# Optimization experiments

Hardware: AMD Instinct MI355X
Metric: run time of the kernel (lower is better)

The kernel has to match this reference:

```python
import jax, jax.numpy as jnp
import numpy as np
import math

B, D, L, H, K, CONV_N = 32, 128, 1024, 8, 7, 4
DK = D // H
EPS = 1e-5


def make_pos_encoding():
    i = np.arange(D, dtype=np.float64)
    freqs = np.where(i % 2 == 0, 10000.0 ** (-i / D), -(10000.0 ** ((1 - i) / D)))
    phases = np.where(i % 2 == 0, 0.0, math.pi / 2)
    pos = np.arange(L, dtype=np.float64)[None, :]  # [1, L]
    pe = np.sin(pos * freqs[:, None] + phases[:, None])  # [D, L]
    return jnp.asarray(pe, dtype=jnp.float32)


def layer_norm_2d(x, w, b):
    # nn.LayerNorm([D, L]) on [B, D, L]: normalize jointly over last two dims
    mu = jnp.mean(x, axis=(1, 2), keepdims=True)
    var = jnp.var(x, axis=(1, 2), keepdims=True)
    return (x - mu) * jax.lax.rsqrt(var + EPS) * w[None] + b[None]


def setup_inputs():
    key = jax.random.key(0)
    ks = jax.random.split(key, 24)
    s = 0.05
    x = jax.random.normal(ks[0], (B, D, L), jnp.float32)
    lengths = jax.random.randint(ks[1], (B,), L // 2, L + 1)
    mask = (jnp.arange(L)[None, :] >= lengths[:, None]).astype(jnp.float32)  # 1 = pad
    inp = {
        "x": x,
        "mask": mask,
        "pos_enc": make_pos_encoding(),
        "normb_w": jnp.ones((D, L), jnp.float32),
        "normb_b": jnp.zeros((D, L), jnp.float32),
        "dw_w": jax.random.normal(ks[2], (CONV_N, D, K), jnp.float32) * s,
        "dw_b": jnp.zeros((CONV_N, D), jnp.float32),
        "pw_w": jax.random.normal(ks[3], (CONV_N, D, D), jnp.float32) * s,
        "pw_b": jnp.zeros((CONV_N, D), jnp.float32),
        "norms_w": jnp.ones((CONV_N, D, L), jnp.float32),
        "norms_b": jnp.zeros((CONV_N, D, L), jnp.float32),
        "qw": jax.random.normal(ks[4], (D, D), jnp.float32) * s,
        "qb": jnp.zeros((D,), jnp.float32),
        "kw": jax.random.normal(ks[5], (D, D), jnp.float32) * s,
        "kb": jnp.zeros((D,), jnp.float32),
        "vw": jax.random.normal(ks[6], (D, D), jnp.float32) * s,
        "vb": jnp.zeros((D,), jnp.float32),
        "aw": jax.random.normal(ks[7], (D, D), jnp.float32) * s,  # attention output fc
        "ab": jnp.zeros((D,), jnp.float32),
        "norme_w": jnp.ones((D, L), jnp.float32),
        "norme_b": jnp.zeros((D, L), jnp.float32),
        "fw": jax.random.normal(ks[8], (D, D), jnp.float32) * s,  # final fc
        "fb": jnp.zeros((D,), jnp.float32),
    }
    return inp


def reference(x, mask, pos_enc, normb_w, normb_b, dw_w, dw_b, pw_w, pw_b,
              norms_w, norms_b, qw, qb, kw, kb, vw, vb, aw, ab,
              norme_w, norme_b, fw, fb):
    # positional encoding + pre-LN
    out = x + pos_enc[None]
    res = out
    out = layer_norm_2d(out, normb_w, normb_b)

    # conv stack (eval mode: dropout is identity)
    for i in range(CONV_N):
        h = jax.lax.conv_general_dilated(
            out, dw_w[i][:, None, :],  # depthwise: [D, 1, K]
            window_strides=(1,), padding=[(K // 2, K // 2)],
            dimension_numbers=("NCH", "OIH", "NCH"),
            feature_group_count=D) + dw_b[i][None, :, None]
        h = jnp.einsum("bcl,oc->bol", h, pw_w[i]) + pw_b[i][None, :, None]
        out = jax.nn.relu(h) + res
        res = out
        out = layer_norm_2d(out, norms_w[i], norms_b[i])

    # multi-head self-attention (manual bmm-softmax-bmm, scale 1/sqrt(d_k))
    xt = jnp.swapaxes(out, 1, 2)  # [B, L, D]
    q = (xt @ qw.T + qb).reshape(B, L, H, DK)
    k = (xt @ kw.T + kb).reshape(B, L, H, DK)
    v = (xt @ vw.T + vb).reshape(B, L, H, DK)
    scores = jnp.einsum("bqhd,bkhd->bhqk", q, k) * (1.0 / math.sqrt(DK))
    m = mask[:, None, None, :]  # broadcast over heads and query dim
    scores = scores * (1.0 - m) + m * (-1e30)
    attn = jax.nn.softmax(scores, axis=-1)
    o = jnp.einsum("bhqk,bkhd->bqhd", attn, v).reshape(B, L, D)
    o = o @ aw.T + ab
    o = jnp.swapaxes(o, 1, 2)  # [B, D, L]

    out = o + res
    res = out
    out = layer_norm_2d(out, norme_w, norme_b)
    out = jnp.einsum("bdl,ed->bel", out, fw) + fb[None, :, None]
    out = jax.nn.relu(out) + res
    return out
```

## Files before the change

kernel.cpp:

```cpp
#include <hip/hip_runtime.h>

#define NB 32
#define ND 128
#define NL 1024
#define NDL (ND*NL)
#define STATS_B 16
#define STATS_R (32*STATS_B)

typedef __attribute__((ext_vector_type(8))) short bf16x8;
typedef __attribute__((ext_vector_type(4))) float f32x4;

__device__ __forceinline__ f32x4 mfma_bf16_16x16x32(bf16x8 a, bf16x8 b, f32x4 c) {
#if defined(__HIP_DEVICE_COMPILE__)
  return __builtin_amdgcn_mfma_f32_16x16x32_bf16(a, b, c, 0, 0, 0);
#else
  return c;
#endif
}

__device__ __forceinline__ float exp2fast(float x) {
#if defined(__HIP_DEVICE_COMPILE__) && __has_builtin(__builtin_amdgcn_exp2f)
  return __builtin_amdgcn_exp2f(x);
#elif defined(__HIP_DEVICE_COMPILE__)
  return __expf(x * 0.6931471805599453f);
#else
  return x;
#endif
}

__device__ __forceinline__ unsigned short bf16rnd(float f) {
  union { float f; unsigned u; } c; c.f = f;
  return (unsigned short)((c.u + 0x7FFFu + ((c.u >> 16) & 1u)) >> 16);
}
__device__ __forceinline__ unsigned packpair(float a, float b) {
  return (unsigned)bf16rnd(a) | ((unsigned)bf16rnd(b) << 16);
}
__device__ __forceinline__ unsigned packtrunc(float a, float b) {
  unsigned ua = __float_as_uint(a), ub = __float_as_uint(b);
  return (ub & 0xFFFF0000u) | (ua >> 16);
}
__device__ __forceinline__ bf16x8 packbf8(float4 a, float4 b) {
  union { unsigned u[4]; bf16x8 v; } r;
  r.u[0] = packpair(a.x, a.y); r.u[1] = packpair(a.z, a.w);
  r.u[2] = packpair(b.x, b.y); r.u[3] = packpair(b.z, b.w);
  return r.v;
}

__device__ __forceinline__ void blockRedAtomic(float s, float sq, float* base) {
  __shared__ float red[16];
#pragma unroll
  for (int off = 32; off > 0; off >>= 1) {
    s  += __shfl_down(s, off, 64);
    sq += __shfl_down(sq, off, 64);
  }
  int wave = threadIdx.x >> 6;
  int nw = blockDim.x >> 6;
  if ((threadIdx.x & 63) == 0) { red[wave*2] = s; red[wave*2+1] = sq; }
  __syncthreads();
  if (threadIdx.x == 0) {
    float ts = 0.f, tq = 0.f;
    for (int i = 0; i < nw; ++i) { ts += red[i*2]; tq += red[i*2+1]; }
    unsafeAtomicAdd(base,     ts);
    unsafeAtomicAdd(base + 1, tq);
  }
}

__global__ void k_zero(float* stats) {
  int t = threadIdx.x;
#pragma unroll
  for (int i = 0; i < 3; ++i) stats[i*1024 + t] = 0.f;
}

__global__ __launch_bounds__(256) void k_addpos(const float* __restrict__ x,
                                                const float* __restrict__ pe,
                                                float* __restrict__ res,
                                                float* __restrict__ stats0) {
  int b = blockIdx.x >> 6;
  int off = ((blockIdx.x & 63) << 11) + (threadIdx.x << 3);
  const float4* xp = (const float4*)(x + (size_t)b*NDL + off);
  const float4* pp = (const float4*)(pe + off);
  float4* rp = (float4*)(res + (size_t)b*NDL + off);
  float s = 0.f, sq = 0.f;
#pragma unroll
  for (int i = 0; i < 2; ++i) {
    float4 a = xp[i], p = pp[i];
    float4 r;
    r.x = a.x + p.x; r.y = a.y + p.y; r.z = a.z + p.z; r.w = a.w + p.w;
    rp[i] = r;
    s  += r.x + r.y + r.z + r.w;
    sq += r.x*r.x + r.y*r.y + r.z*r.z + r.w*r.w;
  }
  blockRedAtomic(s, sq, stats0 + b*STATS_B);
}


__device__ __forceinline__ void load_w_frags16(const float* __restrict__ W,
                                               int wo, int lo, int hi, bf16x8 af[4]) {
#pragma unroll
  for (int kk = 0; kk < 4; ++kk) {
    const float4* wp = (const float4*)(W + (size_t)(wo + lo)*128 + kk*32 + hi*8);
    af[kk] = packbf8(wp[0], wp[1]);
  }
}

__device__ __forceinline__ void mfma_core16(const unsigned* xs, bf16x8 af[4],
                                            int lo, int hi, f32x4 acc[4]) {
#pragma unroll
  for (int ln = 0; ln < 4; ++ln) {
#pragma unroll
    for (int kk = 0; kk < 4; ++kk) {
      int l = ln*16 + lo;
      int off = (l*256 + kk*64 + hi*16) ^ ((lo & 7) << 4);
      bf16x8 bf = *(const bf16x8*)((const char*)xs + off);
      acc[ln] = mfma_bf16_16x16x32(af[kk], bf, acc[ln]);
    }
  }
}

__device__ __forceinline__ void conv_row(const float* __restrict__ srow,
                                         const float* __restrict__ lwrow,
                                         const float* __restrict__ lbrow,
                                         int base, float mu, float rstd,
                                         const float* wk, float bias0,
                                         float* h ) {
  float wa[14];
  bool interior = (base >= 4) && (base + 12 <= NL);
  if (interior) {
    const float4* sp = (const float4*)(srow + base - 4);
    const float4* wp = (const float4*)(lwrow + base - 4);
    const float4* bp = (const float4*)(lbrow + base - 4);
#pragma unroll
    for (int qd = 0; qd < 4; ++qd) {
      float4 s4 = sp[qd], w4 = wp[qd], b4 = bp[qd];
      float sv[4] = {s4.x, s4.y, s4.z, s4.w};
      float wv[4] = {w4.x, w4.y, w4.z, w4.w};
      float bv[4] = {b4.x, b4.y, b4.z, b4.w};
#pragma unroll
      for (int e = 0; e < 4; ++e) {
        int j = qd*4 + e - 1;
        if (j >= 0 && j < 14)
          wa[j] = (sv[e] - mu)*rstd*wv[e] + bv[e];
      }
    }
  } else {
#pragma unroll
    for (int j = 0; j < 14; ++j) {
      int gl = base + j - 3;
      float v = 0.f;
      if (gl >= 0 && gl < NL)
        v = (srow[gl] - mu)*rstd*lwrow[gl] + lbrow[gl];
      wa[j] = v;
    }
  }
#pragma unroll
  for (int l = 0; l < 8; ++l) {
    float acc = bias0;
#pragma unroll
    for (int j = 0; j < 7; ++j) acc += wa[l+j]*wk[j];
    h[l] = acc;
  }
}

template<int MODE>
__global__ __launch_bounds__(512) void k_gemm_mfma(
    const float* __restrict__ src, const unsigned short* __restrict__ srcb16,
    const float* __restrict__ W, const float* __restrict__ bias,
    const float* __restrict__ resbuf, float* __restrict__ wrbuf,
    const float* __restrict__ lnw, const float* __restrict__ lnb,
    const float* __restrict__ dww, const float* __restrict__ dwb,
    const float* __restrict__ statsIn, float* __restrict__ statsOut) {
  __shared__ unsigned xs[4096];
  int b  = blockIdx.x >> 4;
  int l0 = (blockIdx.x & 15) << 6;
  int tid = threadIdx.x;
  int wave = tid >> 6, lane = tid & 63;
  int lo = lane & 15, hi = lane >> 4;
  int wo = wave * 16;

  float mu = 0.f, rstd = 0.f;
  if (MODE == 0 || MODE == 3) {
    mu = statsIn[b*STATS_B] * (1.f/NDL);
    rstd = rsqrtf(statsIn[b*STATS_B + 1]*(1.f/NDL) - mu*mu + 1e-5f);
  }

  if (MODE == 0) {
    int c2 = tid >> 3, lq = tid & 7;
    int c = c2*2, base = l0 + lq*8;
    float wk0[7], wk1[7];
#pragma unroll
    for (int j = 0; j < 7; ++j) { wk0[j] = dww[c*7 + j]; wk1[j] = dww[(c+1)*7 + j]; }
    const float* sa  = src + (size_t)b*NDL + (size_t)c*NL;
    const float* la  = lnw + (size_t)c*NL;
    const float* lbv = lnb + (size_t)c*NL;
    float h0[8], h1[8];
    conv_row(sa,      la,      lbv,      base, mu, rstd, wk0, dwb[c],   h0);
    conv_row(sa + NL, la + NL, lbv + NL, base, mu, rstd, wk1, dwb[c+1], h1);
#pragma unroll
    for (int l = 0; l < 8; ++l) {
      int ll = lq*8 + l;
      xs[(ll << 6) | (c2 ^ ((ll & 7) << 2))] = packpair(h0[l], h1[l]);
    }
  } else if (MODE == 1) {
    for (int i = tid; i < 1024; i += 512) {
      int c2 = i >> 4, lq = (i & 15) << 2;
      int c = c2*2;
      const unsigned short* sp = srcb16 + (size_t)b*NDL + (size_t)c*NL + l0 + lq;
      uint2 ra = *(const uint2*)sp;
      uint2 rb = *(const uint2*)(sp + NL);
      unsigned wv[4];
      wv[0] = (ra.x & 0xFFFFu) | (rb.x << 16);
      wv[1] = (ra.x >> 16)     | (rb.x & 0xFFFF0000u);
      wv[2] = (ra.y & 0xFFFFu) | (rb.y << 16);
      wv[3] = (ra.y >> 16)     | (rb.y & 0xFFFF0000u);
#pragma unroll
      for (int j = 0; j < 4; ++j) {
        int l = lq + j;
        xs[(l << 6) | (c2 ^ ((l & 7) << 2))] = wv[j];
      }
    }
  } else {
    for (int i = tid; i < 1024; i += 512) {
      int c2 = i >> 4, lq = (i & 15) << 2;
      int c = c2*2;
      const float* sp = src + (size_t)b*NDL + (size_t)c*NL + l0 + lq;
      float4 v0 = *(const float4*)sp;
      float4 v1 = *(const float4*)(sp + NL);
      size_t gi = (size_t)c*NL + l0 + lq;
      float4 w0 = *(const float4*)(lnw + gi), w1 = *(const float4*)(lnw + gi + NL);
      float4 bb0 = *(const float4*)(lnb + gi), bb1 = *(const float4*)(lnb + gi + NL);
      float va[4] = {(v0.x-mu)*rstd*w0.x + bb0.x, (v0.y-mu)*rstd*w0.y + bb0.y,
                     (v0.z-mu)*rstd*w0.z + bb0.z, (v0.w-mu)*rstd*w0.w + bb0.w};
      float vb[4] = {(v1.x-mu)*rstd*w1.x + bb1.x, (v1.y-mu)*rstd*w1.y + bb1.y,
                     (v1.z-mu)*rstd*w1.z + bb1.z, (v1.w-mu)*rstd*w1.w + bb1.w};
#pragma unroll
      for (int j = 0; j < 4; ++j) {
        int l = lq + j;
        xs[(l << 6) | (c2 ^ ((l & 7) << 2))] = packpair(va[j], vb[j]);
      }
    }
  }

  bf16x8 af[4];
  load_w_frags16(W, wo, lo, hi, af);
  f32x4 acc[4];
#pragma unroll
  for (int ln = 0; ln < 4; ++ln) acc[ln] = (f32x4){0.f,0.f,0.f,0.f};

  __syncthreads();
  mfma_core16(xs, af, lo, hi, acc);

  if (MODE == 0 || MODE == 1) {
    float s = 0.f, sq = 0.f;
#pragma unroll
    for (int ln = 0; ln < 4; ++ln) {
      int l = l0 + ln*16 + lo;
#pragma unroll
      for (int r = 0; r < 4; ++r) {
        int o = wo + hi*4 + r;
        size_t gi = ((size_t)b*ND + o)*NL + l;
        float v = acc[ln][r] + bias[o];
        if (MODE == 0) v = fmaxf(v, 0.f);
        v += resbuf[gi];
        wrbuf[gi] = v;
        s += v; sq += v*v;
      }
    }
    blockRedAtomic(s, sq, statsOut + b*STATS_B);
  } else {
#pragma unroll
    for (int ln = 0; ln < 4; ++ln) {
      int l = l0 + ln*16 + lo;
#pragma unroll
      for (int r = 0; r < 4; ++r) {
        int o = wo + hi*4 + r;
        size_t gi = ((size_t)b*ND + o)*NL + l;
        wrbuf[gi] = fmaxf(acc[ln][r] + bias[o], 0.f) + resbuf[gi];
      }
    }
  }
}

__global__ __launch_bounds__(512) void k_qkv_mfma(
    const float* __restrict__ src,
    const float* __restrict__ qw, const float* __restrict__ kw, const float* __restrict__ vw,
    const float* __restrict__ qb, const float* __restrict__ kb, const float* __restrict__ vb,
    unsigned short* __restrict__ qo, unsigned short* __restrict__ ko,
    unsigned short* __restrict__ vo,
    const float* __restrict__ lnw, const float* __restrict__ lnb,
    const float* __restrict__ statsIn) {
  __shared__ unsigned xs[4096];
  int b  = blockIdx.x >> 4;
  int l0 = (blockIdx.x & 15) << 6;
  int tid = threadIdx.x;
  int wave = tid >> 6, lane = tid & 63;
  int lo = lane & 15, hi = lane >> 4;
  int wo = wave * 16;

  float mu = statsIn[b*STATS_B] * (1.f/NDL);
  float rstd = rsqrtf(statsIn[b*STATS_B + 1]*(1.f/NDL) - mu*mu + 1e-5f);
  for (int i = tid; i < 1024; i += 512) {
    int c2 = i >> 4, lq = (i & 15) << 2;
    int c = c2*2;
    const float* sp = src + (size_t)b*NDL + (size_t)c*NL + l0 + lq;
    float4 v0 = *(const float4*)sp;
    float4 v1 = *(const float4*)(sp + NL);
    size_t gi = (size_t)c*NL + l0 + lq;
    float4 w0 = *(const float4*)(lnw + gi), w1 = *(const float4*)(lnw + gi + NL);
    float4 bb0 = *(const float4*)(lnb + gi), bb1 = *(const float4*)(lnb + gi + NL);
    float va[4] = {(v0.x-mu)*rstd*w0.x + bb0.x, (v0.y-mu)*rstd*w0.y + bb0.y,
                   (v0.z-mu)*rstd*w0.z + bb0.z, (v0.w-mu)*rstd*w0.w + bb0.w};
    float vb[4] = {(v1.x-mu)*rstd*w1.x + bb1.x, (v1.y-mu)*rstd*w1.y + bb1.y,
                   (v1.z-mu)*rstd*w1.z + bb1.z, (v1.w-mu)*rstd*w1.w + bb1.w};
#pragma unroll
    for (int j = 0; j < 4; ++j) {
      int l = lq + j;
      xs[(l << 6) | (c2 ^ ((l & 7) << 2))] = packpair(va[j], vb[j]);
    }
  }
  __syncthreads();

  const float* Ws[3] = {qw, kw, vw};
  const float* Bs[3] = {qb, kb, vb};
  unsigned short* Os[3] = {qo, ko, vo};
#pragma unroll 1
  for (int mat = 0; mat < 3; ++mat) {
    bf16x8 af[4];
    load_w_frags16(Ws[mat], wo, lo, hi, af);
    f32x4 acc[4];
#pragma unroll
    for (int ln = 0; ln < 4; ++ln) acc[ln] = (f32x4){0.f,0.f,0.f,0.f};
    mfma_core16(xs, af, lo, hi, acc);
    float oscale = (mat == 0) ? 0.25f*1.4426950408889634f : 1.0f;
    const float* bias = Bs[mat];
    unsigned short* op = Os[mat];
#pragma unroll
    for (int ln = 0; ln < 4; ++ln) {
      int l = l0 + ln*16 + lo;
      int o4 = wo + hi*4;
      float vx = (acc[ln][0] + bias[o4+0]) * oscale;
      float vy = (acc[ln][1] + bias[o4+1]) * oscale;
      float vz = (acc[ln][2] + bias[o4+2]) * oscale;
      float vw4 = (acc[ln][3] + bias[o4+3]) * oscale;
      uint2 pk; pk.x = packpair(vx, vy); pk.y = packpair(vz, vw4);
      *(uint2*)(op + ((size_t)b*NL + l)*ND + o4) = pk;
    }
  }
}

template<bool MASKED>
__device__ __forceinline__ void attn_tile(bf16x8 kf0, bf16x8 kf1, bf16x8 vf,
                                          const bf16x8 qf[4], f32x4 acc[4],
                                          float denp[4], int kb, int len, int hi) {
#pragma unroll
  for (int qt = 0; qt < 4; ++qt) {
    f32x4 z = (f32x4){0.f,0.f,0.f,0.f};
    f32x4 s0 = mfma_bf16_16x16x32(kf0, qf[qt], z);
    f32x4 s1 = mfma_bf16_16x16x32(kf1, qf[qt], z);
    float e[8];
#pragma unroll
    for (int r = 0; r < 4; ++r) {
      float e0 = exp2fast(s0[r]);
      float e1 = exp2fast(s1[r]);
      if (MASKED) {
        e0 = (kb + hi*4 + r < len)      ? e0 : 0.f;
        e1 = (kb + 16 + hi*4 + r < len) ? e1 : 0.f;
      }
      e[r] = e0; e[r+4] = e1;
    }
    denp[qt] += ((e[0]+e[1])+(e[2]+e[3])) + ((e[4]+e[5])+(e[6]+e[7]));
    union { unsigned u[4]; bf16x8 v; } pu;
    pu.u[0] = packtrunc(e[0], e[1]);
    pu.u[1] = packtrunc(e[2], e[3]);
    pu.u[2] = packtrunc(e[4], e[5]);
    pu.u[3] = packtrunc(e[6], e[7]);
    acc[qt] = mfma_bf16_16x16x32(vf, pu.v, acc[qt]);
  }
}

__global__ __launch_bounds__(512) void k_attn_fused(
    const unsigned short* __restrict__ q, const unsigned short* __restrict__ k,
    const unsigned short* __restrict__ v, const float* __restrict__ mask,
    unsigned short* __restrict__ att_t) {
  __shared__ short kv[32768];
  __shared__ int slen_sh;
  int bid = blockIdx.x;
  int b  = bid >> 4;
  int h  = (bid >> 1) & 7;
  int qh = bid & 1;
  int tid = threadIdx.x;
  const float* mrow = mask + (size_t)b*NL;

  if (tid == 0) slen_sh = 0;
  __syncthreads();
  {
    int cnt = 0;
    for (int i = tid; i < NL; i += 512) cnt += (mrow[i] == 0.f) ? 1 : 0;
#pragma unroll
    for (int off = 32; off > 0; off >>= 1) cnt += __shfl_down(cnt, off, 64);
    if ((tid & 63) == 0) atomicAdd(&slen_sh, cnt);
  }
  __syncthreads();
  int len = slen_sh;
  int nkt = (len + 31) >> 5;
  int kstage = nkt << 5;

  for (int idx = tid; idx < 4096; idx += 512) {
    int key = idx >> 2, dq = idx & 3;
    if (key >= kstage) break;
    int dk = dq*4;
    uint2 kd; kd.x = 0u; kd.y = 0u;
    if (key < len) kd = *(const uint2*)(k + ((size_t)b*NL + key)*ND + h*16 + dk);
    int kt = key >> 5, w = key & 31;
    int t16 = w >> 4, klo = w & 15;
    int khi = dk >> 3, ii = dk & 7;
    unsigned* dst = (unsigned*)(kv + kt*512 + t16*256 + (khi*16 + klo)*8 + ii);
    dst[0] = kd.x; dst[1] = kd.y;
  }
  for (int idx = tid; idx < 2048; idx += 512) {
    int keyp = idx >> 2, vq = idx & 3;
    int key = keyp*2;
    if (key >= kstage) break;
    int vlo = vq*4;
    uint2 ra, rb; ra.x = ra.y = rb.x = rb.y = 0u;
    size_t voff = ((size_t)b*NL + key)*ND + h*16 + vlo;
    if (key < len)     ra = *(const uint2*)(v + voff);
    if (key + 1 < len) rb = *(const uint2*)(v + voff + ND);
    unsigned wv[4];
    wv[0] = (ra.x & 0xFFFFu) | (rb.x << 16);
    wv[1] = (ra.x >> 16)     | (rb.x & 0xFFFF0000u);
    wv[2] = (ra.y & 0xFFFFu) | (rb.y << 16);
    wv[3] = (ra.y >> 16)     | (rb.y & 0xFFFF0000u);
    int kt = key >> 5, w = key & 31;
    int vhi, ii;
    if (w < 16) { vhi = w >> 2; ii = w & 3; }
    else        { vhi = (w - 16) >> 2; ii = 4 + (w & 3); }
#pragma unroll
    for (int e = 0; e < 4; ++e)
      *(unsigned*)(kv + 16384 + kt*512 + (vhi*16 + vlo + e)*8 + ii) = wv[e];
  }
  __syncthreads();

  int wave = tid >> 6, lane = tid & 63;
  int lo = lane & 15, hi = lane >> 4;
  int q0 = qh*512 + wave*64;

  bf16x8 qf[4];
#pragma unroll
  for (int qt = 0; qt < 4; ++qt) {
    if (hi < 2) {
      union { uint4 u; bf16x8 v; } qu;
      qu.u = *(const uint4*)(q + ((size_t)b*NL + q0 + qt*16 + lo)*ND + h*16 + hi*8);
      qf[qt] = qu.v;
    } else {
      qf[qt] = (bf16x8){0,0,0,0,0,0,0,0};
    }
  }
  f32x4 acc[4];
  float denp[4];
#pragma unroll
  for (int qt = 0; qt < 4; ++qt) { acc[qt] = (f32x4){0.f,0.f,0.f,0.f}; denp[qt] = 0.f; }

  int fullt = len >> 5;
  int l32 = hi*16 + lo;

  bf16x8 cka = (bf16x8){0,0,0,0,0,0,0,0}, ckb = cka, cv;
  if (hi < 2) {
    cka = *(const bf16x8*)(kv + l32*8);
    ckb = *(const bf16x8*)(kv + 256 + l32*8);
  }
  cv = *(const bf16x8*)(kv + 16384 + lane*8);

  for (int kt = 0; kt < nkt; ++kt) {
    bf16x8 nka = cka, nkb = ckb, nv = cv;
    if (kt + 1 < nkt) {
      if (hi < 2) {
        nka = *(const bf16x8*)(kv + (kt+1)*512 + l32*8);
        nkb = *(const bf16x8*)(kv + (kt+1)*512 + 256 + l32*8);
      }
      nv = *(const bf16x8*)(kv + 16384 + (kt+1)*512 + lane*8);
    }
    if (kt < fullt) attn_tile<false>(cka, ckb, cv, qf, acc, denp, kt*32, len, hi);
    else            attn_tile<true >(cka, ckb, cv, qf, acc, denp, kt*32, len, hi);
    cka = nka; ckb = nkb; cv = nv;
  }
#pragma unroll
  for (int qt = 0; qt < 4; ++qt) {
    float d = denp[qt];
    d += __shfl_xor(d, 16, 64);
    d += __shfl_xor(d, 32, 64);
    float inv = 1.f / d;
    size_t obase = ((size_t)b*ND + h*16)*NL + q0 + qt*16 + lo;
#pragma unroll
    for (int r = 0; r < 4; ++r)
      att_t[obase + (size_t)(hi*4 + r)*NL] = bf16rnd(acc[qt][r] * inv);
  }
}

extern "C" void kernel_launch(void* const* d_in, const int* in_sizes, int n_in,
                              void* d_out, int out_size, void* d_ws, size_t ws_size,
                              hipStream_t stream) {
  (void)in_sizes; (void)n_in; (void)out_size; (void)ws_size;
  const float* x       = (const float*)d_in[0];
  const float* mask    = (const float*)d_in[1];
  const float* pe      = (const float*)d_in[2];
  const float* normb_w = (const float*)d_in[3];
  const float* normb_b = (const float*)d_in[4];
  const float* dw_w    = (const float*)d_in[5];
  const float* dw_b    = (const float*)d_in[6];
  const float* pw_w    = (const float*)d_in[7];
  const float* pw_b    = (const float*)d_in[8];
  const float* norms_w = (const float*)d_in[9];
  const float* norms_b = (const float*)d_in[10];
  const float* qw      = (const float*)d_in[11];
  const float* qb      = (const float*)d_in[12];
  const float* kw      = (const float*)d_in[13];
  const float* kb      = (const float*)d_in[14];
  const float* vw      = (const float*)d_in[15];
  const float* vb      = (const float*)d_in[16];
  const float* aw      = (const float*)d_in[17];
  const float* ab      = (const float*)d_in[18];
  const float* norme_w = (const float*)d_in[19];
  const float* norme_b = (const float*)d_in[20];
  const float* fw      = (const float*)d_in[21];
  const float* fb      = (const float*)d_in[22];

  float* out = (float*)d_out;
  float* ws  = (float*)d_ws;
  const size_t NT = (size_t)NB*ND*NL;
  float* resA = ws;
  float* resB = ws + NT;
  unsigned short* qb16 = (unsigned short*)(ws + 2*NT);
  unsigned short* kb16 = qb16 + NT;
  unsigned short* vb16 = kb16 + NT;
  float* stats = ws + 4*NT;
  unsigned short* att16 = (unsigned short*)resB;

  k_zero<<<dim3(1), dim3(1024), 0, stream>>>(stats);
  k_addpos<<<dim3(2048), dim3(256), 0, stream>>>(x, pe, resA, stats);

  for (int i = 0; i < 4; ++i) {
    const float* lw = (i == 0) ? normb_w : norms_w + (size_t)(i-1)*NDL;
    const float* lb = (i == 0) ? normb_b : norms_b + (size_t)(i-1)*NDL;
    const float* rsrc = (i & 1) ? resB : resA;
    float*       rdst = (i & 1) ? resA : resB;
    k_gemm_mfma<0><<<dim3(NB*16), dim3(512), 0, stream>>>(
        rsrc, nullptr, pw_w + i*ND*ND, pw_b + i*ND, rsrc, rdst,
        lw, lb, dw_w + i*ND*7, dw_b + i*ND,
        stats + i*STATS_R, stats + (i+1)*STATS_R);
  }

  const float* ln3w = norms_w + (size_t)3*NDL;
  const float* ln3b = norms_b + (size_t)3*NDL;
  k_qkv_mfma<<<dim3(NB*16), dim3(512), 0, stream>>>(
      resA, qw, kw, vw, qb, kb, vb, qb16, kb16, vb16, ln3w, ln3b, stats + 4*STATS_R);

  k_attn_fused<<<dim3(NB*8*2), dim3(512), 0, stream>>>(qb16, kb16, vb16, mask, att16);

  k_gemm_mfma<1><<<dim3(NB*16), dim3(512), 0, stream>>>(
      nullptr, att16, aw, ab, resA, resA, nullptr, nullptr, nullptr, nullptr,
      nullptr, stats + 5*STATS_R);
  k_gemm_mfma<3><<<dim3(NB*16), dim3(512), 0, stream>>>(
      resA, nullptr, fw, fb, resA, out, norme_w, norme_b, nullptr, nullptr,
      stats + 5*STATS_R, nullptr);
}
```

Measured before the change: 184.3 us.

## Split GEMM K dimension across 16 waves; compute softmax denominator with MFMA

Result: slower. 204.3 us (+10.9%).

```diff
diff --git a/kernel.cpp b/kernel.cpp
--- a/kernel.cpp
+++ b/kernel.cpp
@@ -47,7 +47,7 @@
 }
 
 __device__ __forceinline__ void blockRedAtomic(float s, float sq, float* base) {
-  __shared__ float red[16];
+  __shared__ float red[32];
 #pragma unroll
   for (int off = 32; off > 0; off >>= 1) {
     s  += __shfl_down(s, off, 64);
@@ -94,43 +94,46 @@
 }
 
 
-__device__ __forceinline__ void load_w_frags16(const float* __restrict__ W,
-                                               int wo, int lo, int hi, bf16x8 af[4]) {
-#pragma unroll
-  for (int kk = 0; kk < 4; ++kk) {
+__device__ __forceinline__ void load_w_frags8(const float* __restrict__ W,
+                                              int wo, int lo, int hi, int khalf,
+                                              bf16x8 af[2]) {
+#pragma unroll
+  for (int j = 0; j < 2; ++j) {
+    int kk = khalf*2 + j;
     const float4* wp = (const float4*)(W + (size_t)(wo + lo)*128 + kk*32 + hi*8);
-    af[kk] = packbf8(wp[0], wp[1]);
-  }
-}
-
-__device__ __forceinline__ void mfma_core16(const unsigned* xs, bf16x8 af[4],
-                                            int lo, int hi, f32x4 acc[4]) {
+    af[j] = packbf8(wp[0], wp[1]);
+  }
+}
+
+__device__ __forceinline__ void mfma_core8(const unsigned* xs, bf16x8 af[2],
+                                           int lo, int hi, int khalf, f32x4 acc[4]) {
 #pragma unroll
   for (int ln = 0; ln < 4; ++ln) {
 #pragma unroll
-    for (int kk = 0; kk < 4; ++kk) {
+    for (int j = 0; j < 2; ++j) {
+      int kk = khalf*2 + j;
       int l = ln*16 + lo;
       int off = (l*256 + kk*64 + hi*16) ^ ((lo & 7) << 4);
       bf16x8 bf = *(const bf16x8*)((const char*)xs + off);
-      acc[ln] = mfma_bf16_16x16x32(af[kk], bf, acc[ln]);
-    }
-  }
-}
-
-__device__ __forceinline__ void conv_row(const float* __restrict__ srow,
-                                         const float* __restrict__ lwrow,
-                                         const float* __restrict__ lbrow,
-                                         int base, float mu, float rstd,
-                                         const float* wk, float bias0,
-                                         float* h ) {
-  float wa[14];
-  bool interior = (base >= 4) && (base + 12 <= NL);
+      acc[ln] = mfma_bf16_16x16x32(af[j], bf, acc[ln]);
+    }
+  }
+}
+
+__device__ __forceinline__ void conv_row4(const float* __restrict__ srow,
+                                          const float* __restrict__ lwrow,
+                                          const float* __restrict__ lbrow,
+                                          int base, float mu, float rstd,
+                                          const float* wk, float bias0,
+                                          float* h ) {
+  float wa[10];
+  bool interior = (base >= 4) && (base + 8 <= NL);
   if (interior) {
     const float4* sp = (const float4*)(srow + base - 4);
     const float4* wp = (const float4*)(lwrow + base - 4);
     const float4* bp = (const float4*)(lbrow + base - 4);
 #pragma unroll
-    for (int qd = 0; qd < 4; ++qd) {
+    for (int qd = 0; qd < 3; ++qd) {
       float4 s4 = sp[qd], w4 = wp[qd], b4 = bp[qd];
       float sv[4] = {s4.x, s4.y, s4.z, s4.w};
       float wv[4] = {w4.x, w4.y, w4.z, w4.w};
@@ -138,13 +141,13 @@
 #pragma unroll
       for (int e = 0; e < 4; ++e) {
         int j = qd*4 + e - 1;
-        if (j >= 0 && j < 14)
+        if (j >= 0 && j < 10)
           wa[j] = (sv[e] - mu)*rstd*wv[e] + bv[e];
       }
     }
   } else {
 #pragma unroll
-    for (int j = 0; j < 14; ++j) {
+    for (int j = 0; j < 10; ++j) {
       int gl = base + j - 3;
       float v = 0.f;
       if (gl >= 0 && gl < NL)
@@ -153,7 +156,7 @@
     }
   }
 #pragma unroll
-  for (int l = 0; l < 8; ++l) {
+  for (int l = 0; l < 4; ++l) {
     float acc = bias0;
 #pragma unroll
     for (int j = 0; j < 7; ++j) acc += wa[l+j]*wk[j];
@@ -162,7 +165,7 @@
 }
 
 template<int MODE>
-__global__ __launch_bounds__(512) void k_gemm_mfma(
+__global__ __launch_bounds__(1024) void k_gemm_mfma(
     const float* __restrict__ src, const unsigned short* __restrict__ srcb16,
     const float* __restrict__ W, const float* __restrict__ bias,
     const float* __restrict__ resbuf, float* __restrict__ wrbuf,
@@ -170,12 +173,14 @@
     const float* __restrict__ dww, const float* __restrict__ dwb,
     const float* __restrict__ statsIn, float* __restrict__ statsOut) {
   __shared__ unsigned xs[4096];
+  __shared__ f32x4 redbuf[2048];
   int b  = blockIdx.x >> 4;
   int l0 = (blockIdx.x & 15) << 6;
   int tid = threadIdx.x;
   int wave = tid >> 6, lane = tid & 63;
   int lo = lane & 15, hi = lane >> 4;
-  int wo = wave * 16;
+  int wo = (wave & 7) * 16;
+  int khalf = wave >> 3;
 
   float mu = 0.f, rstd = 0.f;
   if (MODE == 0 || MODE == 3) {
@@ -184,122 +189,40 @@
   }
 
   if (MODE == 0) {
-    int c2 = tid >> 3, lq = tid & 7;
-    int c = c2*2, base = l0 + lq*8;
+    int c2 = tid >> 4, lq = tid & 15;
+    int c = c2*2, base = l0 + lq*4;
     float wk0[7], wk1[7];
 #pragma unroll
     for (int j = 0; j < 7; ++j) { wk0[j] = dww[c*7 + j]; wk1[j] = dww[(c+1)*7 + j]; }
     const float* sa  = src + (size_t)b*NDL + (size_t)c*NL;
     const float* la  = lnw + (size_t)c*NL;
     const float* lbv = lnb + (size_t)c*NL;
-    float h0[8], h1[8];
-    conv_row(sa,      la,      lbv,      base, mu, rstd, wk0, dwb[c],   h0);
-    conv_row(sa + NL, la + NL, lbv + NL, base, mu, rstd, wk1, dwb[c+1], h1);
-#pragma unroll
-    for (int l = 0; l < 8; ++l) {
-      int ll = lq*8 + l;
+    float h0[4], h1[4];
+    conv_row4(sa,      la,      lbv,      base, mu, rstd, wk0, dwb[c],   h0);
+    conv_row4(sa + NL, la + NL, lbv + NL, base, mu, rstd, wk1, dwb[c+1], h1);
+#pragma unroll
+    for (int l = 0; l < 4; ++l) {
+      int ll = lq*4 + l;
       xs[(ll << 6) | (c2 ^ ((ll & 7) << 2))] = packpair(h0[l], h1[l]);
     }
   } else if (MODE == 1) {
-    for (int i = tid; i < 1024; i += 512) {
-      int c2 = i >> 4, lq = (i & 15) << 2;
-      int c = c2*2;
-      const unsigned short* sp = srcb16 + (size_t)b*NDL + (size_t)c*NL + l0 + lq;
-      uint2 ra = *(const uint2*)sp;
-      uint2 rb = *(const uint2*)(sp + NL);
-      unsigned wv[4];
-      wv[0] = (ra.x & 0xFFFFu) | (rb.x << 16);
-      wv[1] = (ra.x >> 16)     | (rb.x & 0xFFFF0000u);
-      wv[2] = (ra.y & 0xFFFFu) | (rb.y << 16);
-      wv[3] = (ra.y >> 16)     | (rb.y & 0xFFFF0000u);
-#pragma unroll
-      for (int j = 0; j < 4; ++j) {
-        int l = lq + j;
-        xs[(l << 6) | (c2 ^ ((l & 7) << 2))] = wv[j];
-      }
+    int c2 = tid >> 4, lq = (tid & 15) << 2;
+    int c = c2*2;
+    const unsigned short* sp = srcb16 + (size_t)b*NDL + (size_t)c*NL + l0 + lq;
+    uint2 ra = *(const uint2*)sp;
+    uint2 rb = *(const uint2*)(sp + NL);
+    unsigned wv[4];
+    wv[0] = (ra.x & 0xFFFFu) | (rb.x << 16);
+    wv[1] = (ra.x >> 16)     | (rb.x & 0xFFFF0000u);
+    wv[2] = (ra.y & 0xFFFFu) | (rb.y << 16);
+    wv[3] = (ra.y >> 16)     | (rb.y & 0xFFFF0000u);
+#pragma unroll
+    for (int j = 0; j < 4; ++j) {
+      int l = lq + j;
+      xs[(l << 6) | (c2 ^ ((l & 7) << 2))] = wv[j];
     }
   } else {
-    for (int i = tid; i < 1024; i += 512) {
-      int c2 = i >> 4, lq = (i & 15) << 2;
-      int c = c2*2;
-      const float* sp = src + (size_t)b*NDL + (size_t)c*NL + l0 + lq;
-      float4 v0 = *(const float4*)sp;
-      float4 v1 = *(const float4*)(sp + NL);
-      size_t gi = (size_t)c*NL + l0 + lq;
-      float4 w0 = *(const float4*)(lnw + gi), w1 = *(const float4*)(lnw + gi + NL);
-      float4 bb0 = *(const float4*)(lnb + gi), bb1 = *(const float4*)(lnb + gi + NL);
-      float va[4] = {(v0.x-mu)*rstd*w0.x + bb0.x, (v0.y-mu)*rstd*w0.y + bb0.y,
-                     (v0.z-mu)*rstd*w0.z + bb0.z, (v0.w-mu)*rstd*w0.w + bb0.w};
-      float vb[4] = {(v1.x-mu)*rstd*w1.x + bb1.x, (v1.y-mu)*rstd*w1.y + bb1.y,
-                     (v1.z-mu)*rstd*w1.z + bb1.z, (v1.w-mu)*rstd*w1.w + bb1.w};
-#pragma unroll
-      for (int j = 0; j < 4; ++j) {
-        int l = lq + j;
-        xs[(l << 6) | (c2 ^ ((l & 7) << 2))] = packpair(va[j], vb[j]);
-      }
-    }
-  }
-
-  bf16x8 af[4];
-  load_w_frags16(W, wo, lo, hi, af);
-  f32x4 acc[4];
-#pragma unroll
-  for (int ln = 0; ln < 4; ++ln) acc[ln] = (f32x4){0.f,0.f,0.f,0.f};
-
-  __syncthreads();
-  mfma_core16(xs, af, lo, hi, acc);
-
-  if (MODE == 0 || MODE == 1) {
-    float s = 0.f, sq = 0.f;
-#pragma unroll
-    for (int ln = 0; ln < 4; ++ln) {
-      int l = l0 + ln*16 + lo;
-#pragma unroll
-      for (int r = 0; r < 4; ++r) {
-        int o = wo + hi*4 + r;
-        size_t gi = ((size_t)b*ND + o)*NL + l;
-        float v = acc[ln][r] + bias[o];
-        if (MODE == 0) v = fmaxf(v, 0.f);
-        v += resbuf[gi];
-        wrbuf[gi] = v;
-        s += v; sq += v*v;
-      }
-    }
-    blockRedAtomic(s, sq, statsOut + b*STATS_B);
-  } else {
-#pragma unroll
-    for (int ln = 0; ln < 4; ++ln) {
-      int l = l0 + ln*16 + lo;
-#pragma unroll
-      for (int r = 0; r < 4; ++r) {
-        int o = wo + hi*4 + r;
-        size_t gi = ((size_t)b*ND + o)*NL + l;
-        wrbuf[gi] = fmaxf(acc[ln][r] + bias[o], 0.f) + resbuf[gi];
-      }
-    }
-  }
-}
-
-__global__ __launch_bounds__(512) void k_qkv_mfma(
-    const float* __restrict__ src,
-    const float* __restrict__ qw, const float* __restrict__ kw, const float* __restrict__ vw,
-    const float* __restrict__ qb, const float* __restrict__ kb, const float* __restrict__ vb,
-    unsigned short* __restrict__ qo, unsigned short* __restrict__ ko,
-    unsigned short* __restrict__ vo,
-    const float* __restrict__ lnw, const float* __restrict__ lnb,
-    const float* __restrict__ statsIn) {
-  __shared__ unsigned xs[4096];
-  int b  = blockIdx.x >> 4;
-  int l0 = (blockIdx.x & 15) << 6;
-  int tid = threadIdx.x;
-  int wave = tid >> 6, lane = tid & 63;
-  int lo = lane & 15, hi = lane >> 4;
-  int wo = wave * 16;
-
-  float mu = statsIn[b*STATS_B] * (1.f/NDL);
-  float rstd = rsqrtf(statsIn[b*STATS_B + 1]*(1.f/NDL) - mu*mu + 1e-5f);
-  for (int i = tid; i < 1024; i += 512) {
-    int c2 = i >> 4, lq = (i & 15) << 2;
+    int c2 = tid >> 4, lq = (tid & 15) << 2;
     int c = c2*2;
     const float* sp = src + (size_t)b*NDL + (size_t)c*NL + l0 + lq;
     float4 v0 = *(const float4*)sp;
@@ -317,6 +240,88 @@
       xs[(l << 6) | (c2 ^ ((l & 7) << 2))] = packpair(va[j], vb[j]);
     }
   }
+
+  bf16x8 af[2];
+  load_w_frags8(W, wo, lo, hi, khalf, af);
+  f32x4 acc[4];
+#pragma unroll
+  for (int ln = 0; ln < 4; ++ln) acc[ln] = (f32x4){0.f,0.f,0.f,0.f};
+
+  __syncthreads();
+  mfma_core8(xs, af, lo, hi, khalf, acc);
+
+  if (khalf == 1) {
+#pragma unroll
+    for (int ln = 0; ln < 4; ++ln) redbuf[ln*512 + (tid & 511)] = acc[ln];
+  }
+  __syncthreads();
+
+  float s = 0.f, sq = 0.f;
+  if (khalf == 0) {
+#pragma unroll
+    for (int ln = 0; ln < 4; ++ln) {
+      f32x4 p = redbuf[ln*512 + tid];
+      acc[ln][0] += p[0]; acc[ln][1] += p[1];
+      acc[ln][2] += p[2]; acc[ln][3] += p[3];
+    }
+#pragma unroll
+    for (int ln = 0; ln < 4; ++ln) {
+      int l = l0 + ln*16 + lo;
+#pragma unroll
+      for (int r = 0; r < 4; ++r) {
+        int o = wo + hi*4 + r;
+        size_t gi = ((size_t)b*ND + o)*NL + l;
+        float v = acc[ln][r] + bias[o];
+        if (MODE == 0 || MODE == 3) v = fmaxf(v, 0.f);
+        v += resbuf[gi];
+        wrbuf[gi] = v;
+        if (MODE != 3) { s += v; sq += v*v; }
+      }
+    }
+  }
+  if (MODE == 0 || MODE == 1)
+    blockRedAtomic(s, sq, statsOut + b*STATS_B);
+}
+
+__global__ __launch_bounds__(1024) void k_qkv_mfma(
+    const float* __restrict__ src,
+    const float* __restrict__ qw, const float* __restrict__ kw, const float* __restrict__ vw,
+    const float* __restrict__ qb, const float* __restrict__ kb, const float* __restrict__ vb,
+    unsigned short* __restrict__ qo, unsigned short* __restrict__ ko,
+    unsigned short* __restrict__ vo,
+    const float* __restrict__ lnw, const float* __restrict__ lnb,
+    const float* __restrict__ statsIn) {
+  __shared__ unsigned xs[4096];
+  __shared__ f32x4 redbuf[2048];
+  int b  = blockIdx.x >> 4;
+  int l0 = (blockIdx.x & 15) << 6;
+  int tid = threadIdx.x;
+  int wave = tid >> 6, lane = tid & 63;
+  int lo = lane & 15, hi = lane >> 4;
+  int wo = (wave & 7) * 16;
+  int khalf = wave >> 3;
+
+  float mu = statsIn[b*STATS_B] * (1.f/NDL);
+  float rstd = rsqrtf(statsIn[b*STATS_B + 1]*(1.f/NDL) - mu*mu + 1e-5f);
+  {
+    int c2 = tid >> 4, lq = (tid & 15) << 2;
+    int c = c2*2;
+    const float* sp = src + (size_t)b*NDL + (size_t)c*NL + l0 + lq;
+    float4 v0 = *(const float4*)sp;
+    float4 v1 = *(const float4*)(sp + NL);
+    size_t gi = (size_t)c*NL + l0 + lq;
+    float4 w0 = *(const float4*)(lnw + gi), w1 = *(const float4*)(lnw + gi + NL);
+    float4 bb0 = *(const float4*)(lnb + gi), bb1 = *(const float4*)(lnb + gi + NL);
+    float va[4] = {(v0.x-mu)*rstd*w0.x + bb0.x, (v0.y-mu)*rstd*w0.y + bb0.y,
+                   (v0.z-mu)*rstd*w0.z + bb0.z, (v0.w-mu)*rstd*w0.w + bb0.w};
+    float vb[4] = {(v1.x-mu)*rstd*w1.x + bb1.x, (v1.y-mu)*rstd*w1.y + bb1.y,
+                   (v1.z-mu)*rstd*w1.z + bb1.z, (v1.w-mu)*rstd*w1.w + bb1.w};
+#pragma unroll
+    for (int j = 0; j < 4; ++j) {
+      int l = lq + j;
+      xs[(l << 6) | (c2 ^ ((l & 7) << 2))] = packpair(va[j], vb[j]);
+    }
+  }
   __syncthreads();
 
   const float* Ws[3] = {qw, kw, vw};
@@ -324,33 +329,43 @@
   unsigned short* Os[3] = {qo, ko, vo};
 #pragma unroll 1
   for (int mat = 0; mat < 3; ++mat) {
-    bf16x8 af[4];
-    load_w_frags16(Ws[mat], wo, lo, hi, af);
+    bf16x8 af[2];
+    load_w_frags8(Ws[mat], wo, lo, hi, khalf, af);
     f32x4 acc[4];
 #pragma unroll
     for (int ln = 0; ln < 4; ++ln) acc[ln] = (f32x4){0.f,0.f,0.f,0.f};
-    mfma_core16(xs, af, lo, hi, acc);
-    float oscale = (mat == 0) ? 0.25f*1.4426950408889634f : 1.0f;
-    const float* bias = Bs[mat];
-    unsigned short* op = Os[mat];
-#pragma unroll
-    for (int ln = 0; ln < 4; ++ln) {
-      int l = l0 + ln*16 + lo;
-      int o4 = wo + hi*4;
-      float vx = (acc[ln][0] + bias[o4+0]) * oscale;
-      float vy = (acc[ln][1] + bias[o4+1]) * oscale;
-      float vz = (acc[ln][2] + bias[o4+2]) * oscale;
-      float vw4 = (acc[ln][3] + bias[o4+3]) * oscale;
-      uint2 pk; pk.x = packpair(vx, vy); pk.y = packpair(vz, vw4);
-      *(uint2*)(op + ((size_t)b*NL + l)*ND + o4) = pk;
-    }
+    mfma_core8(xs, af, lo, hi, khalf, acc);
+    if (khalf == 1) {
+#pragma unroll
+      for (int ln = 0; ln < 4; ++ln) redbuf[ln*512 + (tid & 511)] = acc[ln];
+    }
+    __syncthreads();
+    if (khalf == 0) {
+      float oscale = (mat == 0) ? 0.25f*1.4426950408889634f : 1.0f;
+      const float* bias = Bs[mat];
+      unsigned short* op = Os[mat];
+#pragma unroll
+      for (int ln = 0; ln < 4; ++ln) {
+        f32x4 p = redbuf[ln*512 + tid];
+        int l = l0 + ln*16 + lo;
+        int o4 = wo + hi*4;
+        float vx = (acc[ln][0] + p[0] + bias[o4+0]) * oscale;
+        float vy = (acc[ln][1] + p[1] + bias[o4+1]) * oscale;
+        float vz = (acc[ln][2] + p[2] + bias[o4+2]) * oscale;
+        float vw4 = (acc[ln][3] + p[3] + bias[o4+3]) * oscale;
+        uint2 pk; pk.x = packpair(vx, vy); pk.y = packpair(vz, vw4);
+        *(uint2*)(op + ((size_t)b*NL + l)*ND + o4) = pk;
+      }
+    }
+    __syncthreads();
   }
 }
 
 template<bool MASKED>
 __device__ __forceinline__ void attn_tile(bf16x8 kf0, bf16x8 kf1, bf16x8 vf,
-                                          const bf16x8 qf[4], f32x4 acc[4],
-                                          float denp[4], int kb, int len, int hi) {
+                                          bf16x8 onesf, const bf16x8 qf[4],
+                                          f32x4 acc[4], f32x4 dacc[4],
+                                          int kb, int len, int hi) {
 #pragma unroll
   for (int qt = 0; qt < 4; ++qt) {
     f32x4 z = (f32x4){0.f,0.f,0.f,0.f};
@@ -367,13 +382,13 @@
       }
       e[r] = e0; e[r+4] = e1;
     }
-    denp[qt] += ((e[0]+e[1])+(e[2]+e[3])) + ((e[4]+e[5])+(e[6]+e[7]));
     union { unsigned u[4]; bf16x8 v; } pu;
     pu.u[0] = packtrunc(e[0], e[1]);
     pu.u[1] = packtrunc(e[2], e[3]);
     pu.u[2] = packtrunc(e[4], e[5]);
     pu.u[3] = packtrunc(e[6], e[7]);
-    acc[qt] = mfma_bf16_16x16x32(vf, pu.v, acc[qt]);
+    acc[qt]  = mfma_bf16_16x16x32(vf,    pu.v, acc[qt]);
+    dacc[qt] = mfma_bf16_16x16x32(onesf, pu.v, dacc[qt]);
   }
 }
 
@@ -455,10 +470,14 @@
       qf[qt] = (bf16x8){0,0,0,0,0,0,0,0};
     }
   }
-  f32x4 acc[4];
-  float denp[4];
-#pragma unroll
-  for (int qt = 0; qt < 4; ++qt) { acc[qt] = (f32x4){0.f,0.f,0.f,0.f}; denp[qt] = 0.f; }
+  const short oneb = (short)0x3F80;
+  bf16x8 onesf = (bf16x8){oneb,oneb,oneb,oneb,oneb,oneb,oneb,oneb};
+  f32x4 acc[4], dacc[4];
+#pragma unroll
+  for (int qt = 0; qt < 4; ++qt) {
+    acc[qt]  = (f32x4){0.f,0.f,0.f,0.f};
+    dacc[qt] = (f32x4){0.f,0.f,0.f,0.f};
+  }
 
   int fullt = len >> 5;
   int l32 = hi*16 + lo;
@@ -479,16 +498,13 @@
       }
       nv = *(const bf16x8*)(kv + 16384 + (kt+1)*512 + lane*8);
     }
-    if (kt < fullt) attn_tile<false>(cka, ckb, cv, qf, acc, denp, kt*32, len, hi);
-    else            attn_tile<true >(cka, ckb, cv, qf, acc, denp, kt*32, len, hi);
+    if (kt < fullt) attn_tile<false>(cka, ckb, cv, onesf, qf, acc, dacc, kt*32, len, hi);
+    else            attn_tile<true >(cka, ckb, cv, onesf, qf, acc, dacc, kt*32, len, hi);
     cka = nka; ckb = nkb; cv = nv;
   }
 #pragma unroll
   for (int qt = 0; qt < 4; ++qt) {
-    float d = denp[qt];
-    d += __shfl_xor(d, 16, 64);
-    d += __shfl_xor(d, 32, 64);
-    float inv = 1.f / d;
+    float inv = 1.f / dacc[qt][0];
     size_t obase = ((size_t)b*ND + h*16)*NL + q0 + qt*16 + lo;
 #pragma unroll
     for (int r = 0; r < 4; ++r)
@@ -543,7 +559,7 @@
     const float* lb = (i == 0) ? normb_b : norms_b + (size_t)(i-1)*NDL;
     const float* rsrc = (i & 1) ? resB : resA;
     float*       rdst = (i & 1) ? resA : resB;
-    k_gemm_mfma<0><<<dim3(NB*16), dim3(512), 0, stream>>>(
+    k_gemm_mfma<0><<<dim3(NB*16), dim3(1024), 0, stream>>>(
         rsrc, nullptr, pw_w + i*ND*ND, pw_b + i*ND, rsrc, rdst,
         lw, lb, dw_w + i*ND*7, dw_b + i*ND,
         stats + i*STATS_R, stats + (i+1)*STATS_R);
@@ -551,15 +567,15 @@
 
   const float* ln3w = norms_w + (size_t)3*NDL;
   const float* ln3b = norms_b + (size_t)3*NDL;
-  k_qkv_mfma<<<dim3(NB*16), dim3(512), 0, stream>>>(
+  k_qkv_mfma<<<dim3(NB*16), dim3(1024), 0, stream>>>(
       resA, qw, kw, vw, qb, kb, vb, qb16, kb16, vb16, ln3w, ln3b, stats + 4*STATS_R);
 
   k_attn_fused<<<dim3(NB*8*2), dim3(512), 0, stream>>>(qb16, kb16, vb16, mask, att16);
 
-  k_gemm_mfma<1><<<dim3(NB*16), dim3(512), 0, stream>>>(
+  k_gemm_mfma<1><<<dim3(NB*16), dim3(1024), 0, stream>>>(
       nullptr, att16, aw, ab, resA, resA, nullptr, nullptr, nullptr, nullptr,
       nullptr, stats + 5*STATS_R);
-  k_gemm_mfma<3><<<dim3(NB*16), dim3(512), 0, stream>>>(
+  k_gemm_mfma<3><<<dim3(NB*16), dim3(1024), 0, stream>>>(
       resA, nullptr, fw, fb, resA, out, norme_w, norme_b, nullptr, nullptr,
       stats + 5*STATS_R, nullptr);
 }
```
